# Kernel optimization log

Hardware: AMD Instinct MI355X
Metric: run time of the kernel (lower is better)

Reference implementation:

```python
import jax, jax.numpy as jnp
import numpy as np

B, A_IN, C_IN, H, W_ = 8, 16, 4, 64, 64   # batch, input atoms, input capsules, spatial
K, C_OUT, A_OUT, ROUTINGS = 5, 8, 32, 3
EPS = 1e-7


def setup_inputs() -> dict:
    key = jax.random.key(0)
    k1, k2 = jax.random.split(key)
    x = jax.random.normal(k1, (B, A_IN, C_IN, H, W_), dtype=jnp.float32)
    # kaiming_uniform_(fan_in, relu): bound = sqrt(3) * sqrt(2) / sqrt(fan_in)
    fan_in = A_IN * K * K
    bound = float(np.sqrt(6.0 / fan_in))
    W = jax.random.uniform(k2, (C_OUT * A_OUT, A_IN, K, K), jnp.float32, -bound, bound)
    b = jnp.full((1, 1, C_OUT, A_OUT), 0.1, dtype=jnp.float32)
    return {"x": x, "W": W, "b": b}


def _squash(v):
    # v: (..., atoms); SegCaps squash with epsilon inside sqrt
    sq = jnp.sum(v * v, axis=-1, keepdims=True)
    return v * (sq / (1.0 + sq) / jnp.sqrt(sq + EPS))


def reference(x, W, b):
    # Faithful to torch: permute then raw row-major reshapes (byte reinterpret)
    t = jnp.transpose(x, (2, 0, 3, 4, 1))                      # (C_IN, B, H, W, A_IN)
    t = t.reshape(C_IN * B, H, W_, A_IN).reshape(-1, A_IN, H, W_)
    conv = jax.lax.conv_general_dilated(
        t, W, window_strides=(1, 1), padding="SAME",
        dimension_numbers=("NCHW", "OIHW", "NCHW"))             # (C_IN*B, C_OUT*A_OUT, h, w)
    ch, cw = conv.shape[2], conv.shape[3]
    votes = conv.reshape(B, C_IN, ch, cw, C_OUT, A_OUT)         # raw reinterpret, as in torch
    biases = jnp.tile(b, (ch, cw, 1, 1))                        # (h, w, C_OUT, A_OUT)

    # dynamic routing (SegCaps update_routing)
    logits = jnp.zeros((B, C_IN, ch, cw, C_OUT), dtype=votes.dtype)
    activation = None
    for _ in range(ROUTINGS):
        route = jax.nn.softmax(logits, axis=-1)                 # (B, Cin, h, w, Cout)
        preact = jnp.einsum("bihwo,bihwoa->bhwoa", route, votes) + biases
        activation = _squash(preact)                            # (B, h, w, Cout, A)
        agreement = jnp.einsum("bihwoa,bhwoa->bihwo", votes, activation)
        logits = logits + agreement
    return jnp.transpose(activation, (0, 4, 3, 1, 2))           # (B, A_OUT, C_OUT, h, w)
```

## Files before the change

kernel.cpp:

```cpp
#include <hip/hip_runtime.h>
#include <hip/hip_bf16.h>


typedef _Float16 half8 __attribute__((ext_vector_type(8)));
typedef _Float16 half4v __attribute__((ext_vector_type(4)));
typedef float floatx4 __attribute__((ext_vector_type(4)));

#define EPSF 1e-7f

template <int CTRL>
__device__ __forceinline__ float dppmov(float x) {
  return __int_as_float(__builtin_amdgcn_update_dpp(
      0, __float_as_int(x), CTRL, 0xf, 0xf, false));
}
__device__ __forceinline__ float red_a_add(float x) {
  x += dppmov<0xB1>(x);
  x += dppmov<0x4E>(x);
  x += dppmov<0x141>(x);
  return x;
}
__device__ __forceinline__ float red_o_add(float x) {
  x += dppmov<0x128>(x);
  { float a = x, b = x;
    asm("v_permlane16_swap_b32 %0, %1" : "+v"(a), "+v"(b));
    x = a + b; }
  { float a = x, b = x;
    asm("v_permlane32_swap_b32 %0, %1" : "+v"(a), "+v"(b));
    x = a + b; }
  return x;
}
__device__ __forceinline__ float red_o_max(float x) {
  x = fmaxf(x, dppmov<0x128>(x));
  { float a = x, b = x;
    asm("v_permlane16_swap_b32 %0, %1" : "+v"(a), "+v"(b));
    x = fmaxf(a, b); }
  { float a = x, b = x;
    asm("v_permlane32_swap_b32 %0, %1" : "+v"(a), "+v"(b));
    x = fmaxf(a, b); }
  return x;
}

__global__ __launch_bounds__(1024) void k_pack2(const float* __restrict__ x,
                                                _Float16* __restrict__ th) {
  __shared__ float lin[32 * 306 + 18];
  const int bid = blockIdx.x;
  const int n   = bid >> 3;
  const int a0h = (bid >> 2) & 1;
  const int W0  = (bid & 3) * 16;
  const int ci = n >> 3, b0 = n & 7;
  const int tid = threadIdx.x;
  const float* xb = x + b0 * 262144 + ci * 4096 + W0;

  for (int p = 0; p < 2; ++p) {
    int rr = p * 256 + (tid >> 2);
    int q  = (tid & 3) * 4;
    int a1 = rr >> 5, m = rr & 31;
    float4 v = *(const float4*)(xb + a1 * 16384 + (a0h * 32 + m) * 64 + q);
    float* d = lin + m * 306 + a1 * 18 + q;
    d[0] = v.x; d[1] = v.y; d[2] = v.z; d[3] = v.w;
  }
  __syncthreads();

  _Float16* tb = th + (size_t)n * 65536 + a0h * 32768 + W0 * 128;
  {
    int hh = tid >> 8;
    int w1 = (tid >> 4) & 15;
    int a1 = tid & 15;
    half8 v;
#pragma unroll
    for (int j = 0; j < 8; ++j)
      v[j] = (_Float16)lin[(j * 4 + hh) * 306 + a1 * 18 + w1];
    *(half8*)(tb + hh * 8192 + w1 * 128 + a1 * 8) = v;
  }
}

__global__ __launch_bounds__(256) void k_packw(const float* __restrict__ W,
                                               _Float16* __restrict__ Wp) {
  int id = blockIdx.x * 256 + threadIdx.x;
  int a  = id & 15;
  int oc = (id >> 4) & 255;
  int kk = id >> 12;
  Wp[id] = (kk < 25) ? (_Float16)W[oc * 400 + a * 25 + kk] : (_Float16)0.0f;
}

__global__ __launch_bounds__(512) void k_conv(const _Float16* __restrict__ th,
                                              const _Float16* __restrict__ Wp,
                                              _Float16* __restrict__ votes) {
  __shared__ _Float16 lds[16384];
  const int orig = blockIdx.x;
  const int lid  = (orig & 7) * 256 + (orig >> 3);
  const int y = lid & 63;
  const int n = lid >> 6;
  const int tid = threadIdx.x;

  for (int c = tid; c < 680; c += 512) {
    int a0h = c / 340;
    int rem = c - a0h * 340;
    int r   = rem / 68;
    int col = rem - r * 68;
    int row = y + r - 2;
    half8 v = {};
    if (col >= 2 && col <= 65 && row >= 0 && row < 64)
      v = *(const half8*)(th + (size_t)(((n * 2 + a0h) * 64 + row) * 64 + (col - 2)) * 8);
    *(half8*)(lds + c * 8) = v;
  }
  __syncthreads();

  const int lane  = tid & 63;
  const int wv    = tid >> 6;
  const int col16 = lane & 15;
  const int quad  = lane >> 4;
  const int t     = quad >> 1;
  const int a0h   = quad & 1;
  const int m0    = wv * 32;

  floatx4 acc[2][4] = {};

  const _Float16* wbase = Wp + (size_t)t * 4096 + (m0 + col16) * 16 + a0h * 8;
  const _Float16* lbase = lds + (a0h * 340 + col16) * 8;

  half8 bfc[4], awc[2], bfn[4], awn[2];
  {
    const _Float16* lb = lbase + (t ? 1 : 0) * 8;
#pragma unroll
    for (int xt = 0; xt < 4; ++xt)
      bfc[xt] = *(const half8*)(lb + xt * 128);
#pragma unroll
    for (int oct = 0; oct < 2; ++oct)
      awc[oct] = *(const half8*)(wbase + oct * 256);
  }

#pragma unroll
  for (int s = 0; s < 13; ++s) {
    if (s < 12) {
      const int k0 = 2 * (s + 1);
      const int k1 = (2 * (s + 1) + 1 > 24) ? 24 : 2 * (s + 1) + 1;
      const int e0 = (k0 / 5) * 68 + (k0 % 5);
      const int e1 = (k1 / 5) * 68 + (k1 % 5);
      const _Float16* lb = lbase + (t ? e1 : e0) * 8;
#pragma unroll
      for (int xt = 0; xt < 4; ++xt)
        bfn[xt] = *(const half8*)(lb + xt * 128);
#pragma unroll
      for (int oct = 0; oct < 2; ++oct)
        awn[oct] = *(const half8*)(wbase + (size_t)(s + 1) * 8192 + oct * 256);
    }
#pragma unroll
    for (int oct = 0; oct < 2; ++oct)
#pragma unroll
      for (int xt = 0; xt < 4; ++xt)
        acc[oct][xt] = __builtin_amdgcn_mfma_f32_16x16x32_f16(
            awc[oct], bfc[xt], acc[oct][xt], 0, 0, 0);
    if (s < 12) {
#pragma unroll
      for (int xt = 0; xt < 4; ++xt) bfc[xt] = bfn[xt];
#pragma unroll
      for (int oct = 0; oct < 2; ++oct) awc[oct] = awn[oct];
    }
  }

  __syncthreads();
#pragma unroll
  for (int oct = 0; oct < 2; ++oct)
#pragma unroll
    for (int xt = 0; xt < 4; ++xt)
#pragma unroll
      for (int r = 0; r < 4; ++r) {
        int oc = m0 + oct * 16 + quad * 4 + r;
        int xx = xt * 16 + col16;
        int sw = (oc & 15) >> 1;
        lds[oc * 64 + (xx ^ (sw << 3))] = (_Float16)acc[oct][xt][r];
      }
  __syncthreads();
  _Float16* vb2 = votes + (size_t)n * 1048576 + y * 64;
#pragma unroll
  for (int it = 0; it < 4; ++it) {
    int idx = it * 512 + tid;
    int oc  = idx >> 3;
    int x0  = (idx & 7) << 3;
    int sw  = (oc & 15) >> 1;
    half8 hv = *(const half8*)(lds + oc * 64 + (x0 ^ (sw << 3)));
    *(half8*)(vb2 + (size_t)oc * 4096 + x0) = hv;
  }
}

__global__ __launch_bounds__(256) void k_routing4(
    const _Float16* __restrict__ votes, const float* __restrict__ bias,
    float* __restrict__ out) {
  __shared__ float so[256 * 20];
  const int tid  = threadIdx.x;
  const int lane = tid & 63;
  const int wv   = tid >> 6;
  const int bid  = blockIdx.x;
  const int bv = bid >> 8;
  const int h  = (bid >> 2) & 63;
  const int W0 = (bid & 3) * 16;

  float4 bia = *(const float4*)(bias + lane * 4);
  const int o     = lane >> 3;
  const int a0    = (lane & 7) * 4;
  const int shift = a0 >> 2;
  float bb[4] = {bia.x, bia.y, bia.z, bia.w};

  for (int k = 0; k < 4; ++k) {
    const int wl = wv * 4 + k;
    const int w  = W0 + wl;
    const _Float16* vb = votes + (size_t)bv * 4194304 + h * 16384 + w * 256 + lane * 4;
    float v[4][4];
#pragma unroll
    for (int i = 0; i < 4; ++i) {
      half4v hv = *(const half4v*)(vb + (size_t)i * 1048576);
#pragma unroll
      for (int j = 0; j < 4; ++j) v[i][j] = (float)hv[j];
    }

    float logit[4], act[4], pr[4];

#pragma unroll
    for (int j = 0; j < 4; ++j)
      pr[j] = fmaf(0.125f, (v[0][j] + v[1][j]) + (v[2][j] + v[3][j]), bb[j]);
    {
      float sq = pr[0]*pr[0] + pr[1]*pr[1] + pr[2]*pr[2] + pr[3]*pr[3];
      sq = red_a_add(sq);
      float sc = sq * __builtin_amdgcn_rcpf(1.f + sq)
                    * __builtin_amdgcn_rsqf(sq + EPSF);
#pragma unroll
      for (int j = 0; j < 4; ++j) act[j] = pr[j] * sc;
    }
#pragma unroll
    for (int i = 0; i < 4; ++i) {
      float ag = v[i][0]*act[0] + v[i][1]*act[1] + v[i][2]*act[2] + v[i][3]*act[3];
      logit[i] = red_a_add(ag);
    }

#pragma unroll
    for (int r = 1; r < 3; ++r) {
      float route[4];
#pragma unroll
      for (int i = 0; i < 4; ++i) {
        float m = red_o_max(logit[i]);
        float e = __expf(logit[i] - m);
        float s = red_o_add(e);
        route[i] = e * __builtin_amdgcn_rcpf(s);
      }
#pragma unroll
      for (int j = 0; j < 4; ++j) pr[j] = bb[j];
#pragma unroll
      for (int i = 0; i < 4; ++i)
#pragma unroll
        for (int j = 0; j < 4; ++j)
          pr[j] = fmaf(route[i], v[i][j], pr[j]);
      float sq = pr[0]*pr[0] + pr[1]*pr[1] + pr[2]*pr[2] + pr[3]*pr[3];
      sq = red_a_add(sq);
      float sc = sq * __builtin_amdgcn_rcpf(1.f + sq)
                    * __builtin_amdgcn_rsqf(sq + EPSF);
#pragma unroll
      for (int j = 0; j < 4; ++j) act[j] = pr[j] * sc;
      if (r < 2) {
#pragma unroll
        for (int i = 0; i < 4; ++i) {
          float ag = v[i][0]*act[0] + v[i][1]*act[1] + v[i][2]*act[2] + v[i][3]*act[3];
          logit[i] += red_a_add(ag);
        }
      }
    }

#pragma unroll
    for (int j = 0; j < 4; ++j)
      so[((a0 + j) * 8 + o) * 20 + (wl ^ shift)] = act[j];
  }
  __syncthreads();

  float* ob = out + (size_t)bv * 1048576 + h * 64 + W0;
#pragma unroll
  for (int p = 0; p < 4; ++p) {
    int r  = p * 64 + (tid >> 2);
    int w0 = (tid & 3) * 4;
    int s  = r >> 5;
    float4 tv = *(const float4*)(so + r * 20 + (w0 ^ (s & 4)));
    float tt[4] = {tv.x, tv.y, tv.z, tv.w};
    const int pm = s & 3;
    float4 u = make_float4(tt[0 ^ pm], tt[1 ^ pm], tt[2 ^ pm], tt[3 ^ pm]);
    *(float4*)(ob + (size_t)r * 4096 + w0) = u;
  }
}

extern "C" void kernel_launch(void* const* d_in, const int* in_sizes, int n_in,
                              void* d_out, int out_size, void* d_ws, size_t ws_size,
                              hipStream_t stream) {
  const float* x  = (const float*)d_in[0];
  const float* W  = (const float*)d_in[1];
  const float* b  = (const float*)d_in[2];
  float* out = (float*)d_out;

  _Float16* th    = (_Float16*)d_ws;
  _Float16* Wp    = th + 2097152;
  _Float16* votes = Wp + 106496;

  k_pack2<<<256, 1024, 0, stream>>>(x, th);
  k_packw<<<416, 256, 0, stream>>>(W, Wp);
  k_conv<<<2048, 512, 0, stream>>>(th, Wp, votes);
  k_routing4<<<2048, 256, 0, stream>>>(votes, b, out);
}
```

Before: 131.7 us.

## Remap routing kernel to 8 atoms per lane and one pixel per half-wave

The routing kernel now gives each lane 8 atoms of one output capsule, so a wave covers two pixels and each thread handles a single pixel instead of looping over four. This turns the atom reduction into two DPP steps and the capsule softmax reduction into two DPP steps plus one permlane16 swap, replacing a longer DPP and permlane chain. The grid doubles to 4096 blocks of 8 columns each. The output LDS transpose is shrunk and re-swizzled, so global stores become float2 instead of float4, which may lower store efficiency.

```diff
diff --git a/kernel.cpp b/kernel.cpp
--- a/kernel.cpp
+++ b/kernel.cpp
@@ -5,6 +5,7 @@
 typedef _Float16 half8 __attribute__((ext_vector_type(8)));
 typedef _Float16 half4v __attribute__((ext_vector_type(4)));
 typedef float floatx4 __attribute__((ext_vector_type(4)));
+typedef unsigned uint2v __attribute__((ext_vector_type(2)));
 
 #define EPSF 1e-7f
 
@@ -13,31 +14,24 @@
   return __int_as_float(__builtin_amdgcn_update_dpp(
       0, __float_as_int(x), CTRL, 0xf, 0xf, false));
 }
-__device__ __forceinline__ float red_a_add(float x) {
+__device__ __forceinline__ float red_g_add(float x) {
   x += dppmov<0xB1>(x);
   x += dppmov<0x4E>(x);
-  x += dppmov<0x141>(x);
   return x;
 }
-__device__ __forceinline__ float red_o_add(float x) {
+__device__ __forceinline__ float red_o2_add(float x) {
+  x += dppmov<0x124>(x);
   x += dppmov<0x128>(x);
-  { float a = x, b = x;
-    asm("v_permlane16_swap_b32 %0, %1" : "+v"(a), "+v"(b));
-    x = a + b; }
-  { float a = x, b = x;
-    asm("v_permlane32_swap_b32 %0, %1" : "+v"(a), "+v"(b));
-    x = a + b; }
-  return x;
-}
-__device__ __forceinline__ float red_o_max(float x) {
+  uint2v r = __builtin_amdgcn_permlane16_swap(
+      __float_as_uint(x), __float_as_uint(x), false, false);
+  return __uint_as_float(r[0]) + __uint_as_float(r[1]);
+}
+__device__ __forceinline__ float red_o2_max(float x) {
+  x = fmaxf(x, dppmov<0x124>(x));
   x = fmaxf(x, dppmov<0x128>(x));
-  { float a = x, b = x;
-    asm("v_permlane16_swap_b32 %0, %1" : "+v"(a), "+v"(b));
-    x = fmaxf(a, b); }
-  { float a = x, b = x;
-    asm("v_permlane32_swap_b32 %0, %1" : "+v"(a), "+v"(b));
-    x = fmaxf(a, b); }
-  return x;
+  uint2v r = __builtin_amdgcn_permlane16_swap(
+      __float_as_uint(x), __float_as_uint(x), false, false);
+  return fmaxf(__uint_as_float(r[0]), __uint_as_float(r[1]));
 }
 
 __global__ __launch_bounds__(1024) void k_pack2(const float* __restrict__ x,
@@ -184,104 +178,114 @@
   }
 }
 
-__global__ __launch_bounds__(256) void k_routing4(
+__global__ __launch_bounds__(256) void k_routing9(
     const _Float16* __restrict__ votes, const float* __restrict__ bias,
     float* __restrict__ out) {
-  __shared__ float so[256 * 20];
+  __shared__ float so[256 * 9];
   const int tid  = threadIdx.x;
   const int lane = tid & 63;
   const int wv   = tid >> 6;
   const int bid  = blockIdx.x;
-  const int bv = bid >> 8;
-  const int h  = (bid >> 2) & 63;
-  const int W0 = (bid & 3) * 16;
-
-  float4 bia = *(const float4*)(bias + lane * 4);
-  const int o     = lane >> 3;
-  const int a0    = (lane & 7) * 4;
-  const int shift = a0 >> 2;
-  float bb[4] = {bia.x, bia.y, bia.z, bia.w};
-
-  for (int k = 0; k < 4; ++k) {
-    const int wl = wv * 4 + k;
-    const int w  = W0 + wl;
-    const _Float16* vb = votes + (size_t)bv * 4194304 + h * 16384 + w * 256 + lane * 4;
-    float v[4][4];
+  const int bv = bid >> 9;
+  const int h  = (bid >> 3) & 63;
+  const int W0 = (bid & 7) * 8;
+
+  const int half = lane >> 5;
+  const int o    = (lane >> 2) & 7;
+  const int g    = lane & 3;
+  const int col  = wv * 2 + half;
+  const int w    = W0 + col;
+
+  float bb[8];
+  {
+    const float4 b0 = *(const float4*)(bias + o * 32 + g * 8);
+    const float4 b1 = *(const float4*)(bias + o * 32 + g * 8 + 4);
+    bb[0]=b0.x; bb[1]=b0.y; bb[2]=b0.z; bb[3]=b0.w;
+    bb[4]=b1.x; bb[5]=b1.y; bb[6]=b1.z; bb[7]=b1.w;
+  }
+
+  const _Float16* vb = votes + (size_t)bv * 4194304 + h * 16384 + w * 256
+                     + o * 32 + g * 8;
+  float v[4][8];
+#pragma unroll
+  for (int i = 0; i < 4; ++i) {
+    half8 hv = *(const half8*)(vb + (size_t)i * 1048576);
+#pragma unroll
+    for (int j = 0; j < 8; ++j) v[i][j] = (float)hv[j];
+  }
+
+  float logit[4], act[8], pr[8];
+
+#pragma unroll
+  for (int j = 0; j < 8; ++j)
+    pr[j] = fmaf(0.125f, (v[0][j] + v[1][j]) + (v[2][j] + v[3][j]), bb[j]);
+  {
+    float sq = pr[0]*pr[0];
+#pragma unroll
+    for (int j = 1; j < 8; ++j) sq = fmaf(pr[j], pr[j], sq);
+    sq = red_g_add(sq);
+    float sc = sq * __builtin_amdgcn_rcpf(1.f + sq)
+                  * __builtin_amdgcn_rsqf(sq + EPSF);
+#pragma unroll
+    for (int j = 0; j < 8; ++j) act[j] = pr[j] * sc;
+  }
+#pragma unroll
+  for (int i = 0; i < 4; ++i) {
+    float ag = v[i][0] * act[0];
+#pragma unroll
+    for (int j = 1; j < 8; ++j) ag = fmaf(v[i][j], act[j], ag);
+    logit[i] = red_g_add(ag);
+  }
+
+#pragma unroll
+  for (int r = 1; r < 3; ++r) {
+    float route[4];
 #pragma unroll
     for (int i = 0; i < 4; ++i) {
-      half4v hv = *(const half4v*)(vb + (size_t)i * 1048576);
-#pragma unroll
-      for (int j = 0; j < 4; ++j) v[i][j] = (float)hv[j];
+      float m = red_o2_max(logit[i]);
+      float e = __expf(logit[i] - m);
+      float s = red_o2_add(e);
+      route[i] = e * __builtin_amdgcn_rcpf(s);
     }
-
-    float logit[4], act[4], pr[4];
-
-#pragma unroll
-    for (int j = 0; j < 4; ++j)
-      pr[j] = fmaf(0.125f, (v[0][j] + v[1][j]) + (v[2][j] + v[3][j]), bb[j]);
-    {
-      float sq = pr[0]*pr[0] + pr[1]*pr[1] + pr[2]*pr[2] + pr[3]*pr[3];
-      sq = red_a_add(sq);
-      float sc = sq * __builtin_amdgcn_rcpf(1.f + sq)
-                    * __builtin_amdgcn_rsqf(sq + EPSF);
-#pragma unroll
-      for (int j = 0; j < 4; ++j) act[j] = pr[j] * sc;
-    }
-#pragma unroll
-    for (int i = 0; i < 4; ++i) {
-      float ag = v[i][0]*act[0] + v[i][1]*act[1] + v[i][2]*act[2] + v[i][3]*act[3];
-      logit[i] = red_a_add(ag);
-    }
-
-#pragma unroll
-    for (int r = 1; r < 3; ++r) {
-      float route[4];
+#pragma unroll
+    for (int j = 0; j < 8; ++j) pr[j] = bb[j];
+#pragma unroll
+    for (int i = 0; i < 4; ++i)
+#pragma unroll
+      for (int j = 0; j < 8; ++j)
+        pr[j] = fmaf(route[i], v[i][j], pr[j]);
+    float sq = pr[0]*pr[0];
+#pragma unroll
+    for (int j = 1; j < 8; ++j) sq = fmaf(pr[j], pr[j], sq);
+    sq = red_g_add(sq);
+    float sc = sq * __builtin_amdgcn_rcpf(1.f + sq)
+                  * __builtin_amdgcn_rsqf(sq + EPSF);
+#pragma unroll
+    for (int j = 0; j < 8; ++j) act[j] = pr[j] * sc;
+    if (r < 2) {
 #pragma unroll
       for (int i = 0; i < 4; ++i) {
-        float m = red_o_max(logit[i]);
-        float e = __expf(logit[i] - m);
-        float s = red_o_add(e);
-        route[i] = e * __builtin_amdgcn_rcpf(s);
-      }
-#pragma unroll
-      for (int j = 0; j < 4; ++j) pr[j] = bb[j];
-#pragma unroll
-      for (int i = 0; i < 4; ++i)
-#pragma unroll
-        for (int j = 0; j < 4; ++j)
-          pr[j] = fmaf(route[i], v[i][j], pr[j]);
-      float sq = pr[0]*pr[0] + pr[1]*pr[1] + pr[2]*pr[2] + pr[3]*pr[3];
-      sq = red_a_add(sq);
-      float sc = sq * __builtin_amdgcn_rcpf(1.f + sq)
-                    * __builtin_amdgcn_rsqf(sq + EPSF);
-#pragma unroll
-      for (int j = 0; j < 4; ++j) act[j] = pr[j] * sc;
-      if (r < 2) {
-#pragma unroll
-        for (int i = 0; i < 4; ++i) {
-          float ag = v[i][0]*act[0] + v[i][1]*act[1] + v[i][2]*act[2] + v[i][3]*act[3];
-          logit[i] += red_a_add(ag);
-        }
+        float ag = v[i][0] * act[0];
+#pragma unroll
+        for (int j = 1; j < 8; ++j) ag = fmaf(v[i][j], act[j], ag);
+        logit[i] += red_g_add(ag);
       }
     }
-
-#pragma unroll
-    for (int j = 0; j < 4; ++j)
-      so[((a0 + j) * 8 + o) * 20 + (wl ^ shift)] = act[j];
-  }
+  }
+
+#pragma unroll
+  for (int j = 0; j < 8; ++j)
+    so[(g * 64 + j * 8 + o) * 9 + (col ^ g)] = act[j];
   __syncthreads();
 
   float* ob = out + (size_t)bv * 1048576 + h * 64 + W0;
 #pragma unroll
   for (int p = 0; p < 4; ++p) {
     int r  = p * 64 + (tid >> 2);
-    int w0 = (tid & 3) * 4;
-    int s  = r >> 5;
-    float4 tv = *(const float4*)(so + r * 20 + (w0 ^ (s & 4)));
-    float tt[4] = {tv.x, tv.y, tv.z, tv.w};
-    const int pm = s & 3;
-    float4 u = make_float4(tt[0 ^ pm], tt[1 ^ pm], tt[2 ^ pm], tt[3 ^ pm]);
-    *(float4*)(ob + (size_t)r * 4096 + w0) = u;
+    int c2 = (tid & 3) * 2;
+    float lo = so[r * 9 + (c2 ^ p)];
+    float hi = so[r * 9 + ((c2 + 1) ^ p)];
+    *(float2*)(ob + (size_t)r * 4096 + c2) = make_float2(lo, hi);
   }
 }
 
@@ -300,5 +304,5 @@
   k_pack2<<<256, 1024, 0, stream>>>(x, th);
   k_packw<<<416, 256, 0, stream>>>(W, Wp);
   k_conv<<<2048, 512, 0, stream>>>(th, Wp, votes);
-  k_routing4<<<2048, 256, 0, stream>>>(votes, b, out);
-}
+  k_routing9<<<4096, 256, 0, stream>>>(votes, b, out);
+}
```

Result: faster. 129.0 us (-2.1%).
